# Performance work log

Measured on AMD Instinct MI355X. Metric: run time of the kernel, lower is better.

## Reference

```python
import jax, jax.numpy as jnp
import numpy as np


def sparsemax(z):
    # sparsemax along the last axis (matches tfa.activations.sparsemax default axis=-1)
    K = z.shape[-1]
    zs = -jnp.sort(-z, axis=-1)                      # descending sort
    cs = jnp.cumsum(zs, axis=-1)
    k = jnp.arange(1, K + 1, dtype=z.dtype)
    support = 1.0 + k * zs > cs                      # support set indicator
    kmax = jnp.sum(support, axis=-1, keepdims=True)  # |support|, int
    cs_k = jnp.take_along_axis(cs, kmax - 1, axis=-1)
    tau = (cs_k - 1.0) / kmax.astype(z.dtype)
    return jnp.maximum(z - tau, 0.0)


def binary_lut(depth):
    # (depth, 2**depth, 2) table mapping leaf index -> per-level bit / complement
    idx = np.arange(2 ** depth)
    off = 2 ** np.arange(depth)
    bits = (idx[None, :] // off[:, None]) % 2        # (depth, 2**depth)
    return jnp.asarray(np.stack([bits, 1 - bits], axis=-1), dtype=jnp.float32)


def setup_inputs() -> dict:
    key = jax.random.key(0)
    ks = jax.random.split(key, 5)
    B, F, N, D, U = 8192, 256, 128, 6, 16
    return {
        "x": jax.random.normal(ks[0], (B, F), dtype=jnp.float32),
        "feature_selection_logits": jax.random.normal(ks[1], (F, N, D), dtype=jnp.float32),
        "feature_thresholds": jax.random.normal(ks[2], (N, D), dtype=jnp.float32),
        "log_temperatures": jax.random.normal(ks[3], (N, D), dtype=jnp.float32) * 0.1,
        "response": jax.random.normal(ks[4], (N, U, 2 ** D), dtype=jnp.float32),
        "depth": D,
    }


def reference(x, feature_selection_logits, feature_thresholds, log_temperatures, response, depth):
    lut = binary_lut(depth)                                          # (d, 2**d, 2)
    selectors = sparsemax(feature_selection_logits)                  # (i, n, d)
    fv = jnp.einsum('bi,ind->bnd', x, selectors)                     # (b, n, d)
    tl = (fv - feature_thresholds) * jnp.exp(-log_temperatures)      # (b, n, d)
    tl = jnp.stack([-tl, tl], axis=-1)                               # (b, n, d, 2)
    gates = jnp.clip(0.5 * tl + 0.5, 0.0, 1.0)                       # sparsemoid
    rg = jnp.einsum('bnds,dcs->bndc', gates, lut)                    # (b, n, d, 2**d)
    rg = jnp.prod(rg, axis=-2)                                       # (b, n, 2**d)
    resp = jnp.einsum('bnc,nuc->bnu', rg, response)                  # (b, n, u)
    return jnp.mean(resp, axis=1)                                    # (b, u)
```

## Files before the change

kernel.cpp:

```cpp
#include <hip/hip_runtime.h>
#include <hip/hip_bf16.h>


typedef float f32x4 __attribute__((ext_vector_type(4)));
typedef unsigned int u32;
typedef _Float16 h16;
typedef _Float16 h16x2 __attribute__((ext_vector_type(2)));
typedef _Float16 h16x8 __attribute__((ext_vector_type(8)));

#define WPF_OFF   0
#define RESPF_OFF 393216
#define BIAS_OFF  655360

#define GLD    776
#define GLROWB (GLD * 2)

union h2u { h16x2 h; u32 u; };
union hbits { h16 h; unsigned short s; };
union fragh { u32 w[4]; h16x8 v; int4 i4; h16x2 h2[4]; };

__device__ inline unsigned short h16r(float f) {
    hbits t; t.h = (h16)f; return t.s;
}
__device__ inline u32 packh2(float a, float b) {
    h2u t; t.h[0] = (h16)a; t.h[1] = (h16)b; return t.u;
}

__device__ inline f32x4 mfma_f16(h16x8 a, h16x8 b, f32x4 c) {
    return __builtin_amdgcn_mfma_f32_16x16x32_f16(a, b, c, 0, 0, 0);
}

__global__ __launch_bounds__(256) void k_prep(const float* __restrict__ fsl,
                                              const float* __restrict__ thr,
                                              const float* __restrict__ logt,
                                              const float* __restrict__ resp,
                                              unsigned short* __restrict__ WpF,
                                              unsigned short* __restrict__ respF,
                                              float* __restrict__ bias) {
    int bb  = blockIdx.x;
    int tid = threadIdx.x;
    if (bb < 128) {
        __shared__ unsigned short sm[8][192];
        int ib = (bb & 31) * 8;
        int nb = (bb >> 5) * 32;
        int il = tid >> 5;
        int nl = tid & 31;
        int i = ib + il;
        int n = nb + nl;
        const float* zp = fsl + (i * 128 + n) * 6;

        float z[6], zs[6];
        #pragma unroll
        for (int d = 0; d < 6; ++d) { z[d] = zp[d]; zs[d] = z[d]; }
        #pragma unroll
        for (int a = 0; a < 5; ++a) {
            #pragma unroll
            for (int b = a + 1; b < 6; ++b) {
                float hi = fmaxf(zs[a], zs[b]);
                float lo = fminf(zs[a], zs[b]);
                zs[a] = hi; zs[b] = lo;
            }
        }
        float cs = 0.f, csel = 0.f;
        int   km = 1;
        #pragma unroll
        for (int k = 0; k < 6; ++k) {
            cs += zs[k];
            if (1.0f + (float)(k + 1) * zs[k] > cs) { km = k + 1; csel = cs; }
        }
        float tau = (csel - 1.0f) / (float)km;

        #pragma unroll
        for (int d = 0; d < 6; ++d) {
            float invT = expf(-logt[n * 6 + d]);
            float sel  = fmaxf(z[d] - tau, 0.0f);
            float wv   = sel * 0.5f * invT;
            sm[il][nl * 6 + d] = h16r(wv);
            if (i == 0) bias[n * 6 + d] = 0.5f - 0.5f * invT * thr[n * 6 + d];
        }
        __syncthreads();

        if (tid < 192) {
            int ct  = (nb * 6) / 16 + (tid >> 4);
            int clm = tid & 15;
            int kt  = ib >> 5;
            int lq  = (ib >> 3) & 3;
            union { unsigned short s[8]; int4 i4; } o;
            #pragma unroll
            for (int j = 0; j < 8; ++j) o.s[j] = sm[j][tid];
            *(int4*)(WpF + (size_t)(((ct * 8 + kt) * 64 + lq * 16 + clm) * 8)) = o.i4;
        }
    } else {
        int t = (bb - 128) * 256 + tid;
        int n  = t >> 7;
        int k2 = (t >> 6) & 1;
        int l  = t & 63;
        int u  = l & 15;
        int c0 = k2 * 32 + (l >> 4) * 8;
        const float* rp = resp + n * 1024 + u * 64 + c0;
        float4 ra = *(const float4*)rp;
        float4 rb = *(const float4*)(rp + 4);
        int4 o;
        o.x = (int)packh2(ra.x, ra.y);
        o.y = (int)packh2(ra.z, ra.w);
        o.z = (int)packh2(rb.x, rb.y);
        o.w = (int)packh2(rb.z, rb.w);
        ((int4*)respF)[(n * 2 + k2) * 64 + l] = o;
    }
}

__global__ __launch_bounds__(1024, 4) void k_main(const float* __restrict__ x,
                                                  const unsigned short* __restrict__ WpF,
                                                  const unsigned short* __restrict__ respF,
                                                  const float* __restrict__ bias,
                                                  float* __restrict__ out) {
    __shared__ char smemraw[49664];
    unsigned short* gl = (unsigned short*)smemraw;
    float* lds2 = (float*)smemraw;
    const int4* xf = (const int4*)smemraw;

    int tid = threadIdx.x;
    int w  = tid >> 6;
    int l  = tid & 63;
    int cl = l & 15;
    int lq = l >> 4;
    int rowbase = blockIdx.x * 32;
    int ntbase  = w * 3;

    {
        int k8  = tid & 31;
        int row = tid >> 5;
        const float* xp = x + (size_t)(rowbase + row) * 256 + k8 * 8;
        float4 xa = *(const float4*)(xp);
        float4 xb = *(const float4*)(xp + 4);
        int4 p;
        p.x = (int)packh2(xa.x, xa.y);
        p.y = (int)packh2(xa.z, xa.w);
        p.z = (int)packh2(xb.x, xb.y);
        p.w = (int)packh2(xb.z, xb.w);
        int rt = row >> 4, rl = row & 15, kt = k8 >> 2, klq = k8 & 3;
        char* basep = smemraw + (size_t)(rt * 8 + kt) * 1024
                              + (size_t)(((klq * 16 + rl) ^ kt) * 16);
        *(int4*)basep = p;
    }
    __syncthreads();

    f32x4 acc[3][2];
    #pragma unroll
    for (int j = 0; j < 3; ++j) {
        acc[j][0] = (f32x4){0.f, 0.f, 0.f, 0.f};
        acc[j][1] = (f32x4){0.f, 0.f, 0.f, 0.f};
    }
    const int4* wp4 = (const int4*)WpF;

    #pragma unroll
    for (int kt = 0; kt < 8; ++kt) {
        fragh b[3];
        #pragma unroll
        for (int j = 0; j < 3; ++j)
            b[j].i4 = wp4[((ntbase + j) * 8 + kt) * 64 + l];
        #pragma unroll
        for (int rt = 0; rt < 2; ++rt) {
            fragh ah;
            ah.i4 = xf[(rt * 8 + kt) * 64 + (l ^ kt)];
            #pragma unroll
            for (int j = 0; j < 3; ++j)
                acc[j][rt] = mfma_f16(ah.v, b[j].v, acc[j][rt]);
        }
    }
    __syncthreads();

    #pragma unroll
    for (int j = 0; j < 3; ++j) {
        int col = (ntbase + j) * 16 + cl;
        float bv = bias[col];
        #pragma unroll
        for (int rt = 0; rt < 2; ++rt) {
            #pragma unroll
            for (int r = 0; r < 4; ++r) {
                float g = acc[j][rt][r] + bv;
                g = fminf(fmaxf(g, 0.f), 1.f);
                int row = rt * 16 + lq * 4 + r;
                gl[row * GLD + col] = h16r(g);
            }
        }
    }
    __syncthreads();

    f32x4 oacc0 = (f32x4){0.f, 0.f, 0.f, 0.f};
    f32x4 oacc1 = (f32x4){0.f, 0.f, 0.f, 0.f};
    const int4* rp4 = (const int4*)respF;
    int treebase = w * 8;
    const h16x2 onev = (h16x2){(h16)1.0f, (h16)1.0f};

    #pragma unroll 2
    for (int t2 = 0; t2 < 8; ++t2) {
        int n = treebase + t2;
        fragh rb0, rb1;
        rb0.i4 = rp4[(n * 2 + 0) * 64 + l];
        rb1.i4 = rp4[(n * 2 + 1) * 64 + l];
        #pragma unroll
        for (int rt = 0; rt < 2; ++rt) {
            int row = rt * 16 + cl;
            const u32* gp = (const u32*)((const char*)gl + row * GLROWB + n * 12);
            h2u g01u, g23u, g45u;
            g01u.u = gp[0]; g23u.u = gp[1]; g45u.u = gp[2];
            h16x2 g01 = g01u.h, g23 = g23u.h, g45 = g45u.h;
            h16x2 s01 = onev - g01;
            h16x2 s23 = onev - g23;
            h16x2 s45 = onev - g45;
            h16x2 gs0  = __builtin_shufflevector(g01, s01, 0, 2);
            h16x2 b1g  = __builtin_shufflevector(g01, g01, 1, 1);
            h16x2 b1s  = __builtin_shufflevector(s01, s01, 1, 1);
            h16x2 t01a = gs0 * b1g;
            h16x2 t01b = gs0 * b1s;
            h16x2 g2b  = __builtin_shufflevector(g23, g23, 0, 0);
            h16x2 s2b  = __builtin_shufflevector(s23, s23, 0, 0);
            h16x2 pa01 = t01a * g2b;
            h16x2 pa23 = t01b * g2b;
            h16x2 pa45 = t01a * s2b;
            h16x2 pa67 = t01b * s2b;
            h16 f3  = (lq & 1) ? s23[1] : g23[1];
            h16 f4  = (lq & 2) ? s45[0] : g45[0];
            h16 m34 = f3 * f4;
            h16 pbl = m34 * g45[1];
            h16 pbh = m34 * s45[1];
            h16x2 pblb = (h16x2){pbl, pbl};
            h16x2 pbhb = (h16x2){pbh, pbh};
            fragh fa1, fa2;
            fa1.h2[0] = pa01 * pblb; fa1.h2[1] = pa23 * pblb;
            fa1.h2[2] = pa45 * pblb; fa1.h2[3] = pa67 * pblb;
            fa2.h2[0] = pa01 * pbhb; fa2.h2[1] = pa23 * pbhb;
            fa2.h2[2] = pa45 * pbhb; fa2.h2[3] = pa67 * pbhb;
            if (rt == 0) {
                oacc0 = mfma_f16(fa1.v, rb0.v, oacc0);
                oacc0 = mfma_f16(fa2.v, rb1.v, oacc0);
            } else {
                oacc1 = mfma_f16(fa1.v, rb0.v, oacc1);
                oacc1 = mfma_f16(fa2.v, rb1.v, oacc1);
            }
        }
    }
    __syncthreads();

    #pragma unroll
    for (int r = 0; r < 4; ++r) {
        lds2[(w * 2 + 0) * 272 + (lq * 4 + r) * 17 + cl] = oacc0[r];
        lds2[(w * 2 + 1) * 272 + (lq * 4 + r) * 17 + cl] = oacc1[r];
    }
    __syncthreads();
    if (tid < 512) {
        int r = tid >> 4, u = tid & 15;
        int rt = r >> 4, ri = r & 15;
        float s = 0.f;
        #pragma unroll
        for (int ww = 0; ww < 16; ++ww)
            s += lds2[(ww * 2 + rt) * 272 + ri * 17 + u];
        out[(size_t)(rowbase + r) * 16 + u] = s * (1.0f / 128.0f);
    }
}

extern "C" void kernel_launch(void* const* d_in, const int* in_sizes, int n_in,
                              void* d_out, int out_size, void* d_ws, size_t ws_size,
                              hipStream_t stream) {
    (void)in_sizes; (void)n_in; (void)out_size; (void)ws_size;
    const float* x    = (const float*)d_in[0];
    const float* fsl  = (const float*)d_in[1];
    const float* thr  = (const float*)d_in[2];
    const float* logt = (const float*)d_in[3];
    const float* resp = (const float*)d_in[4];

    char* ws = (char*)d_ws;
    unsigned short* WpF   = (unsigned short*)(ws + WPF_OFF);
    unsigned short* respF = (unsigned short*)(ws + RESPF_OFF);
    float*          bias  = (float*)(ws + BIAS_OFF);
    float* out = (float*)d_out;

    k_prep<<<192, 256, 0, stream>>>(fsl, thr, logt, resp, WpF, respF, bias);
    k_main<<<256, 1024, 0, stream>>>(x, WpF, respF, bias, out);
}
```

Measured before the change: 21.72 us.

## Split trees across two half-blocks and combine partial outputs with atomics

Each 32-row tile is now handled by two 512-thread blocks, each owning half of the 128 trees. This doubles the grid to 512 blocks and shrinks the per-block gate buffer in shared memory. Partial means are combined with atomicAdd into an output that is zeroed first by a memset. The cost is an extra memset launch, atomic traffic, x loaded twice (once per half-block), and nondeterministic float summation order.

```diff
diff --git a/kernel.cpp b/kernel.cpp
--- a/kernel.cpp
+++ b/kernel.cpp
@@ -12,8 +12,8 @@
 #define RESPF_OFF 393216
 #define BIAS_OFF  655360
 
-#define GLD    776
-#define GLROWB (GLD * 2)
+#define GLD2    392
+#define GLROWB2 (GLD2 * 2)
 
 union h2u { h16x2 h; u32 u; };
 union hbits { h16 h; unsigned short s; };
@@ -109,27 +109,32 @@
     }
 }
 
-__global__ __launch_bounds__(1024, 4) void k_main(const float* __restrict__ x,
-                                                  const unsigned short* __restrict__ WpF,
-                                                  const unsigned short* __restrict__ respF,
-                                                  const float* __restrict__ bias,
-                                                  float* __restrict__ out) {
-    __shared__ char smemraw[49664];
-    unsigned short* gl = (unsigned short*)smemraw;
+__global__ __launch_bounds__(512, 4) void k_main(const float* __restrict__ x,
+                                                 const unsigned short* __restrict__ WpF,
+                                                 const unsigned short* __restrict__ respF,
+                                                 const float* __restrict__ bias,
+                                                 float* __restrict__ out) {
+    __shared__ char smemraw[16384 + 25088];
+    char* xfraw = smemraw;
+    unsigned short* gl = (unsigned short*)(smemraw + 16384);
     float* lds2 = (float*)smemraw;
-    const int4* xf = (const int4*)smemraw;
+    const int4* xf4 = (const int4*)smemraw;
 
     int tid = threadIdx.x;
     int w  = tid >> 6;
     int l  = tid & 63;
     int cl = l & 15;
     int lq = l >> 4;
-    int rowbase = blockIdx.x * 32;
-    int ntbase  = w * 3;
-
-    {
-        int k8  = tid & 31;
-        int row = tid >> 5;
+    int rowbase = (blockIdx.x >> 1) * 32;
+    int th      = blockIdx.x & 1;
+    int ctbase  = th * 24 + w * 3;
+    int nbase   = th * 64;
+
+    #pragma unroll
+    for (int it = 0; it < 2; ++it) {
+        int a   = it * 512 + tid;
+        int k8  = a & 31;
+        int row = a >> 5;
         const float* xp = x + (size_t)(rowbase + row) * 256 + k8 * 8;
         float4 xa = *(const float4*)(xp);
         float4 xb = *(const float4*)(xp + 4);
@@ -139,8 +144,8 @@
         p.z = (int)packh2(xb.x, xb.y);
         p.w = (int)packh2(xb.z, xb.w);
         int rt = row >> 4, rl = row & 15, kt = k8 >> 2, klq = k8 & 3;
-        char* basep = smemraw + (size_t)(rt * 8 + kt) * 1024
-                              + (size_t)(((klq * 16 + rl) ^ kt) * 16);
+        char* basep = xfraw + (size_t)(rt * 8 + kt) * 1024
+                            + (size_t)(((klq * 16 + rl) ^ kt) * 16);
         *(int4*)basep = p;
     }
     __syncthreads();
@@ -158,22 +163,22 @@
         fragh b[3];
         #pragma unroll
         for (int j = 0; j < 3; ++j)
-            b[j].i4 = wp4[((ntbase + j) * 8 + kt) * 64 + l];
+            b[j].i4 = wp4[((ctbase + j) * 8 + kt) * 64 + l];
         #pragma unroll
         for (int rt = 0; rt < 2; ++rt) {
             fragh ah;
-            ah.i4 = xf[(rt * 8 + kt) * 64 + (l ^ kt)];
+            ah.i4 = xf4[(rt * 8 + kt) * 64 + (l ^ kt)];
             #pragma unroll
             for (int j = 0; j < 3; ++j)
                 acc[j][rt] = mfma_f16(ah.v, b[j].v, acc[j][rt]);
         }
     }
-    __syncthreads();
 
     #pragma unroll
     for (int j = 0; j < 3; ++j) {
-        int col = (ntbase + j) * 16 + cl;
-        float bv = bias[col];
+        int colg = (ctbase + j) * 16 + cl;
+        int coll = (w * 3 + j) * 16 + cl;
+        float bv = bias[colg];
         #pragma unroll
         for (int rt = 0; rt < 2; ++rt) {
             #pragma unroll
@@ -181,7 +186,7 @@
                 float g = acc[j][rt][r] + bv;
                 g = fminf(fmaxf(g, 0.f), 1.f);
                 int row = rt * 16 + lq * 4 + r;
-                gl[row * GLD + col] = h16r(g);
+                gl[row * GLD2 + coll] = h16r(g);
             }
         }
     }
@@ -190,19 +195,19 @@
     f32x4 oacc0 = (f32x4){0.f, 0.f, 0.f, 0.f};
     f32x4 oacc1 = (f32x4){0.f, 0.f, 0.f, 0.f};
     const int4* rp4 = (const int4*)respF;
-    int treebase = w * 8;
     const h16x2 onev = (h16x2){(h16)1.0f, (h16)1.0f};
 
     #pragma unroll 2
     for (int t2 = 0; t2 < 8; ++t2) {
-        int n = treebase + t2;
+        int nloc = w * 8 + t2;
+        int n    = nbase + nloc;
         fragh rb0, rb1;
         rb0.i4 = rp4[(n * 2 + 0) * 64 + l];
         rb1.i4 = rp4[(n * 2 + 1) * 64 + l];
         #pragma unroll
         for (int rt = 0; rt < 2; ++rt) {
             int row = rt * 16 + cl;
-            const u32* gp = (const u32*)((const char*)gl + row * GLROWB + n * 12);
+            const u32* gp = (const u32*)((const char*)gl + row * GLROWB2 + nloc * 12);
             h2u g01u, g23u, g45u;
             g01u.u = gp[0]; g23u.u = gp[1]; g45u.u = gp[2];
             h16x2 g01 = g01u.h, g23 = g23u.h, g45 = g45u.h;
@@ -241,29 +246,28 @@
             }
         }
     }
+
+    #pragma unroll
+    for (int r = 0; r < 4; ++r) {
+        lds2[(w * 2 + 0) * 256 + (lq * 4 + r) * 16 + cl] = oacc0[r];
+        lds2[(w * 2 + 1) * 256 + (lq * 4 + r) * 16 + cl] = oacc1[r];
+    }
     __syncthreads();
-
-    #pragma unroll
-    for (int r = 0; r < 4; ++r) {
-        lds2[(w * 2 + 0) * 272 + (lq * 4 + r) * 17 + cl] = oacc0[r];
-        lds2[(w * 2 + 1) * 272 + (lq * 4 + r) * 17 + cl] = oacc1[r];
-    }
-    __syncthreads();
-    if (tid < 512) {
+    {
         int r = tid >> 4, u = tid & 15;
         int rt = r >> 4, ri = r & 15;
         float s = 0.f;
         #pragma unroll
-        for (int ww = 0; ww < 16; ++ww)
-            s += lds2[(ww * 2 + rt) * 272 + ri * 17 + u];
-        out[(size_t)(rowbase + r) * 16 + u] = s * (1.0f / 128.0f);
+        for (int ww = 0; ww < 8; ++ww)
+            s += lds2[(ww * 2 + rt) * 256 + ri * 16 + u];
+        atomicAdd(&out[(size_t)(rowbase + r) * 16 + u], s * (1.0f / 128.0f));
     }
 }
 
 extern "C" void kernel_launch(void* const* d_in, const int* in_sizes, int n_in,
                               void* d_out, int out_size, void* d_ws, size_t ws_size,
                               hipStream_t stream) {
-    (void)in_sizes; (void)n_in; (void)out_size; (void)ws_size;
+    (void)in_sizes; (void)n_in; (void)ws_size;
     const float* x    = (const float*)d_in[0];
     const float* fsl  = (const float*)d_in[1];
     const float* thr  = (const float*)d_in[2];
@@ -276,6 +280,7 @@
     float*          bias  = (float*)(ws + BIAS_OFF);
     float* out = (float*)d_out;
 
+    hipMemsetAsync(d_out, 0, (size_t)out_size * sizeof(float), stream);
     k_prep<<<192, 256, 0, stream>>>(fsl, thr, logt, resp, WpF, respF, bias);
-    k_main<<<256, 1024, 0, stream>>>(x, WpF, respF, bias, out);
-}
+    k_main<<<512, 512, 0, stream>>>(x, WpF, respF, bias, out);
+}
```

After: 22.96 us. 1.06x slower.

## Keep gates wave-local in LDS to drop block-wide barriers

Applied to the files above, without the earlier changes.

Each wave now writes its 48 gate columns (its own 8 trees × 6 depths) into a private LDS slice and reads them back for the tree-product MFMA stage. This removes two __syncthreads between the GEMM, gate and response phases. The per-wave partial outputs are stored in the same private region with a rotated column index to avoid bank conflicts, which removes another barrier before the cross-wave reduction. LDS use grows to 64 KB per block, which could limit occupancy.

```diff
diff --git a/kernel.cpp b/kernel.cpp
--- a/kernel.cpp
+++ b/kernel.cpp
@@ -1,5 +1,4 @@
 #include <hip/hip_runtime.h>
-#include <hip/hip_bf16.h>
 
 
 typedef float f32x4 __attribute__((ext_vector_type(4)));
@@ -11,9 +10,6 @@
 #define WPF_OFF   0
 #define RESPF_OFF 393216
 #define BIAS_OFF  655360
-
-#define GLD    776
-#define GLROWB (GLD * 2)
 
 union h2u { h16x2 h; u32 u; };
 union hbits { h16 h; unsigned short s; };
@@ -114,10 +110,8 @@
                                                   const unsigned short* __restrict__ respF,
                                                   const float* __restrict__ bias,
                                                   float* __restrict__ out) {
-    __shared__ char smemraw[49664];
-    unsigned short* gl = (unsigned short*)smemraw;
-    float* lds2 = (float*)smemraw;
-    const int4* xf = (const int4*)smemraw;
+    __shared__ char smemraw[65536];
+    const int4* xf4 = (const int4*)smemraw;
 
     int tid = threadIdx.x;
     int w  = tid >> 6;
@@ -125,7 +119,9 @@
     int cl = l & 15;
     int lq = l >> 4;
     int rowbase = blockIdx.x * 32;
-    int ntbase  = w * 3;
+    int ctbase  = w * 3;
+
+    unsigned short* gw = (unsigned short*)(smemraw + 16384 + w * 3072);
 
     {
         int k8  = tid & 31;
@@ -158,22 +154,22 @@
         fragh b[3];
         #pragma unroll
         for (int j = 0; j < 3; ++j)
-            b[j].i4 = wp4[((ntbase + j) * 8 + kt) * 64 + l];
+            b[j].i4 = wp4[((ctbase + j) * 8 + kt) * 64 + l];
         #pragma unroll
         for (int rt = 0; rt < 2; ++rt) {
             fragh ah;
-            ah.i4 = xf[(rt * 8 + kt) * 64 + (l ^ kt)];
+            ah.i4 = xf4[(rt * 8 + kt) * 64 + (l ^ kt)];
             #pragma unroll
             for (int j = 0; j < 3; ++j)
                 acc[j][rt] = mfma_f16(ah.v, b[j].v, acc[j][rt]);
         }
     }
-    __syncthreads();
 
     #pragma unroll
     for (int j = 0; j < 3; ++j) {
-        int col = (ntbase + j) * 16 + cl;
-        float bv = bias[col];
+        int colg = (ctbase + j) * 16 + cl;
+        int coll = j * 16 + cl;
+        float bv = bias[colg];
         #pragma unroll
         for (int rt = 0; rt < 2; ++rt) {
             #pragma unroll
@@ -181,28 +177,26 @@
                 float g = acc[j][rt][r] + bv;
                 g = fminf(fmaxf(g, 0.f), 1.f);
                 int row = rt * 16 + lq * 4 + r;
-                gl[row * GLD + col] = h16r(g);
+                gw[row * 48 + coll] = h16r(g);
             }
         }
     }
-    __syncthreads();
 
     f32x4 oacc0 = (f32x4){0.f, 0.f, 0.f, 0.f};
     f32x4 oacc1 = (f32x4){0.f, 0.f, 0.f, 0.f};
     const int4* rp4 = (const int4*)respF;
-    int treebase = w * 8;
     const h16x2 onev = (h16x2){(h16)1.0f, (h16)1.0f};
 
     #pragma unroll 2
     for (int t2 = 0; t2 < 8; ++t2) {
-        int n = treebase + t2;
+        int n = w * 8 + t2;
         fragh rb0, rb1;
         rb0.i4 = rp4[(n * 2 + 0) * 64 + l];
         rb1.i4 = rp4[(n * 2 + 1) * 64 + l];
         #pragma unroll
         for (int rt = 0; rt < 2; ++rt) {
             int row = rt * 16 + cl;
-            const u32* gp = (const u32*)((const char*)gl + row * GLROWB + n * 12);
+            const u32* gp = (const u32*)((const char*)gw + row * 96 + t2 * 12);
             h2u g01u, g23u, g45u;
             g01u.u = gp[0]; g23u.u = gp[1]; g45u.u = gp[2];
             h16x2 g01 = g01u.h, g23 = g23u.h, g45 = g45u.h;
@@ -241,21 +235,25 @@
             }
         }
     }
+
+    {
+        float* pw = (float*)(smemraw + 16384 + w * 3072);
+        int us = (cl + w) & 15;
+        #pragma unroll
+        for (int r = 0; r < 4; ++r) {
+            pw[(lq * 4 + r) * 16 + us]        = oacc0[r];
+            pw[(16 + lq * 4 + r) * 16 + us]   = oacc1[r];
+        }
+    }
     __syncthreads();
 
-    #pragma unroll
-    for (int r = 0; r < 4; ++r) {
-        lds2[(w * 2 + 0) * 272 + (lq * 4 + r) * 17 + cl] = oacc0[r];
-        lds2[(w * 2 + 1) * 272 + (lq * 4 + r) * 17 + cl] = oacc1[r];
-    }
-    __syncthreads();
     if (tid < 512) {
         int r = tid >> 4, u = tid & 15;
-        int rt = r >> 4, ri = r & 15;
+        const float* pb = (const float*)(smemraw + 16384);
         float s = 0.f;
         #pragma unroll
         for (int ww = 0; ww < 16; ++ww)
-            s += lds2[(ww * 2 + rt) * 272 + ri * 17 + u];
+            s += pb[ww * 768 + r * 16 + ((u + ww) & 15)];
         out[(size_t)(rowbase + r) * 16 + u] = s * (1.0f / 128.0f);
     }
 }
```

Measured after the change: 20.90 us. 3.8% less time.
